# Kernel optimization log

Hardware: AMD Instinct MI355X
Metric: run time of the kernel (lower is better)

Reference implementation:

```python
import jax, jax.numpy as jnp
import numpy as np

# Video-DiT scale: d_model = H * D = 2048
B, S_T, S_C, H, D = 2, 2048, 1024, 16, 128


def setup_inputs() -> dict:
    key = jax.random.key(0)
    ks = jax.random.split(key, 6)
    f = lambda k, s: jax.random.normal(k, s, dtype=jnp.float32)
    return {
        "target_q": f(ks[0], (B, S_T, H, D)),
        "target_k": f(ks[1], (B, S_T, H, D)),
        "target_v": f(ks[2], (B, S_T, H, D)),
        "cond_k": f(ks[3], (B, S_C, H, D)),
        "cond_v": f(ks[4], (B, S_C, H, D)),
        "b_param": f(ks[5], (1,)),
    }


def reference(target_q, target_k, target_v, cond_k, cond_v, b_param):
    """Extended target self-attention over [target_k; cond_k] with a scalar
    logit bias b_param added only to the condition-key columns.
    Inputs BSHD; returns [B, S_t, H*D] (ready for output_proj)."""
    Bq, St, Hh, Dd = target_q.shape
    Sc = cond_k.shape[1]
    scale = Dd ** -0.5  # softmax_scale defaults to head_dim**-0.5

    k_ext = jnp.concatenate([target_k, cond_k], axis=1)  # [B, S_t+S_c, H, D]
    v_ext = jnp.concatenate([target_v, cond_v], axis=1)

    # [B, H, S_t, S_t+S_c]
    logits = jnp.einsum('bqhd,bkhd->bhqk', target_q, k_ext) * jnp.asarray(scale, target_q.dtype)
    # bias: 0 on target keys, b on cond keys
    bias = jnp.concatenate([
        jnp.zeros((St,), logits.dtype),
        jnp.broadcast_to(b_param.astype(logits.dtype), (Sc,)),
    ])
    logits = logits + bias[None, None, None, :]

    probs = jax.nn.softmax(logits, axis=-1)
    out = jnp.einsum('bhqk,bkhd->bqhd', probs, v_ext)  # [B, S_t, H, D]
    return out.reshape(Bq, St, Hh * Dd)
```

## Files before the change

kernel.cpp:

```cpp
#include <hip/hip_runtime.h>
#include <hip/hip_bf16.h>

typedef __attribute__((ext_vector_type(4))) float f32x4;
typedef __attribute__((ext_vector_type(16))) float f32x16;
typedef __attribute__((ext_vector_type(8))) short bf8;
typedef __attribute__((ext_vector_type(2))) int i32x2;

#define B_ 2
#define ST 2048
#define SC 1024
#define SK 3072
#define NH 16
#define DH 128
#define KVB 32
#define NT 96
#define TGT 64
#define SCALE 0.088388347648318447f
#define LOG2E 1.4426950408889634f

__device__ __forceinline__ i32x2 tr_read(unsigned a) {
    i32x2 d;
    asm volatile("ds_read_b64_tr_b16 %0, %1" : "=v"(d) : "v"(a));
    return d;
}

__device__ __forceinline__ unsigned cvtpk(float lo, float hi) {
    unsigned r;
    asm("v_cvt_pk_bf16_f32 %0, %1, %2" : "=v"(r) : "v"(lo), "v"(hi));
    return r;
}

__device__ __forceinline__ void swap32(unsigned &a, unsigned &b) {
    asm volatile("v_permlane32_swap_b32 %0, %1" : "+v"(a), "+v"(b));
}

__device__ __forceinline__ bf8 mk_bf8(i32x2 a, i32x2 b) {
    union { i32x2 h[2]; bf8 v; } u;
    u.h[0] = a; u.h[1] = b;
    return u.v;
}
__device__ __forceinline__ bf8 mk_bf8w(unsigned w0, unsigned w1, unsigned w2, unsigned w3) {
    union { unsigned w[4]; bf8 v; } u;
    u.w[0] = w0; u.w[1] = w1; u.w[2] = w2; u.w[3] = w3;
    return u.v;
}
__device__ __forceinline__ bf8 pack_bf8(f32x4 a, f32x4 b) {
    return mk_bf8w(cvtpk(a[0], a[1]), cvtpk(a[2], a[3]),
                   cvtpk(b[0], b[1]), cvtpk(b[2], b[3]));
}

__global__ __launch_bounds__(256, 2)
void attn_fwd(const float* __restrict__ Q,
              const float* __restrict__ TK,
              const float* __restrict__ TV,
              const float* __restrict__ CK,
              const float* __restrict__ CV,
              const float* __restrict__ BP,
              float* __restrict__ OUT)
{
    __shared__ __align__(16) unsigned short Ks[2][KVB * DH];
    __shared__ __align__(16) unsigned short Vs[2][KVB * DH];

    const int tid = threadIdx.x;
    const int w   = tid >> 6;
    const int l   = tid & 63;
    const int r31 = l & 31;
    const int hi  = l >> 5;

    const int bid = blockIdx.x;
    const int xcd = bid & 7;
    const int sub = bid >> 3;
    const int bh  = xcd * 4 + (sub >> 4);
    const int qt  = sub & 15;
    const int bb  = bh >> 4;
    const int hh  = bh & 15;

    const float biasl = BP[0] * LOG2E;

    const int qrow = qt * 128 + w * 32 + r31;
    const float* qp = Q + (((size_t)bb * ST + qrow) * NH + hh) * DH;
    const float qsc = SCALE * LOG2E;
    bf8 qf[8];
#pragma unroll
    for (int dk = 0; dk < 8; ++dk) {
        const f32x4 x0 = *(const f32x4*)(qp + dk * 16 + hi * 8);
        const f32x4 x1 = *(const f32x4*)(qp + dk * 16 + hi * 8 + 4);
        qf[dk] = mk_bf8w(cvtpk(x0[0]*qsc, x0[1]*qsc), cvtpk(x0[2]*qsc, x0[3]*qsc),
                         cvtpk(x1[0]*qsc, x1[1]*qsc), cvtpk(x1[2]*qsc, x1[3]*qsc));
    }

    f32x16 oa[4];
#pragma unroll
    for (int dt = 0; dt < 4; ++dt)
#pragma unroll
        for (int e = 0; e < 16; ++e) oa[dt][e] = 0.f;
    float l_run = 0.f;

    f32x4 skr[2][2], svr[2][2];

    auto stage_load = [&](int t) {
        const int kv0 = t * KVB;
        const float *kb, *vb;
        if (kv0 < ST) {
            const size_t off = (((size_t)bb * ST + kv0) * NH + hh) * DH;
            kb = TK + off; vb = TV + off;
        } else {
            const size_t off = (((size_t)bb * SC + (kv0 - ST)) * NH + hh) * DH;
            kb = CK + off; vb = CV + off;
        }
#pragma unroll
        for (int i = 0; i < 2; ++i) {
            const int c = tid + (i << 8);
            const int krow = c >> 4;
            const int kcol = ((c & 15) ^ (krow & 7)) << 3;
            const float* kp = kb + (size_t)krow * (NH * DH) + kcol;
            skr[i][0] = *(const f32x4*)kp;
            skr[i][1] = *(const f32x4*)(kp + 4);
            const int vkv = (((c >> 8) & 1) << 4) | (((c >> 4) & 1) << 3)
                          | (((c >> 7) & 1) << 2) | ((c >> 1) & 3);
            const int vd  = (((c >> 5) & 3) << 5) | (((c >> 3) & 1) << 4)
                          | ((c & 1) << 3);
            const float* vp = vb + (size_t)vkv * (NH * DH) + vd;
            svr[i][0] = *(const f32x4*)vp;
            svr[i][1] = *(const f32x4*)(vp + 4);
        }
    };

    auto stage_write = [&](int buf) {
#pragma unroll
        for (int i = 0; i < 2; ++i) {
            const int c = tid + (i << 8);
            *(bf8*)((char*)Ks[buf] + c * 16) = pack_bf8(skr[i][0], skr[i][1]);
            *(bf8*)((char*)Vs[buf] + c * 16) = pack_bf8(svr[i][0], svr[i][1]);
        }
    };

    stage_load(0);
    stage_write(0);

    const unsigned vLane = (unsigned)(size_t)&Vs[0][0]
                         + (unsigned)((l >> 4) * 128 + (l & 15) * 8);

    for (int t = 0; t < NT; ++t) {
        __syncthreads();
        if (t + 1 < NT) stage_load(t + 1);
        const int buf = t & 1;
        const float bias = (t >= TGT) ? biasl : 0.f;

        f32x16 s0;
#pragma unroll
        for (int e = 0; e < 16; ++e) s0[e] = bias;
        __builtin_amdgcn_s_setprio(1);
#pragma unroll
        for (int dk = 0; dk < 8; ++dk) {
            int o = r31 * 256 + (dk * 16 + hi * 8) * 2;
            o ^= (r31 & 7) << 4;
            const bf8 kf = *(const bf8*)((const char*)Ks[buf] + o);
            s0 = __builtin_amdgcn_mfma_f32_32x32x16_bf16(kf, qf[dk], s0, 0, 0, 0);
        }
        __builtin_amdgcn_s_setprio(0);

        asm volatile("" ::: "memory");
        const unsigned vA = vLane + (unsigned)(buf << 13);
        i32x2 vt_[2][4][2];
#pragma unroll
        for (int ks = 0; ks < 2; ++ks) {
            const unsigned vk = vA + (unsigned)(ks << 12);
#pragma unroll
            for (int dt = 0; dt < 4; ++dt) {
                vt_[ks][dt][0] = tr_read(vk + dt * 512);
                vt_[ks][dt][1] = tr_read(vk + dt * 512 + 2048);
            }
        }

        if (t + 1 < NT) stage_write(buf ^ 1);

        float rs = 0.f;
#pragma unroll
        for (int e = 0; e < 16; ++e) {
            s0[e] = __builtin_amdgcn_exp2f(s0[e]);
            rs += s0[e];
        }
        l_run += rs;

        unsigned a0 = cvtpk(s0[0], s0[1]),  b0 = cvtpk(s0[4], s0[5]);
        unsigned a1 = cvtpk(s0[2], s0[3]),  b1 = cvtpk(s0[6], s0[7]);
        swap32(a0, b0); swap32(a1, b1);
        const bf8 pf0 = mk_bf8w(a0, a1, b0, b1);
        unsigned a2 = cvtpk(s0[8], s0[9]),   b2 = cvtpk(s0[12], s0[13]);
        unsigned a3 = cvtpk(s0[10], s0[11]), b3 = cvtpk(s0[14], s0[15]);
        swap32(a2, b2); swap32(a3, b3);
        const bf8 pf1 = mk_bf8w(a2, a3, b2, b3);

        asm volatile("s_waitcnt lgkmcnt(0)");
        __builtin_amdgcn_sched_barrier(0);
        __builtin_amdgcn_s_setprio(1);
#pragma unroll
        for (int ks = 0; ks < 2; ++ks) {
            const bf8 pf = ks ? pf1 : pf0;
#pragma unroll
            for (int dt = 0; dt < 4; ++dt) {
                const bf8 vf = mk_bf8(vt_[ks][dt][0], vt_[ks][dt][1]);
                oa[dt] = __builtin_amdgcn_mfma_f32_32x32x16_bf16(vf, pf, oa[dt], 0, 0, 0);
            }
        }
        __builtin_amdgcn_s_setprio(0);
    }

    const float l_tot = l_run + __shfl_xor(l_run, 32);
    const float inv = 1.0f / l_tot;
    float* op = OUT + ((size_t)(bb * ST + qrow)) * (NH * DH) + hh * DH;
#pragma unroll
    for (int dt = 0; dt < 4; ++dt)
#pragma unroll
        for (int rr = 0; rr < 4; ++rr) {
            f32x4 st;
            st[0] = oa[dt][rr * 4 + 0] * inv;
            st[1] = oa[dt][rr * 4 + 1] * inv;
            st[2] = oa[dt][rr * 4 + 2] * inv;
            st[3] = oa[dt][rr * 4 + 3] * inv;
            *(f32x4*)(op + dt * 32 + rr * 8 + hi * 4) = st;
        }
}

extern "C" void kernel_launch(void* const* d_in, const int* in_sizes, int n_in,
                              void* d_out, int out_size, void* d_ws, size_t ws_size,
                              hipStream_t stream) {
    const float* q  = (const float*)d_in[0];
    const float* tk = (const float*)d_in[1];
    const float* tv = (const float*)d_in[2];
    const float* ck = (const float*)d_in[3];
    const float* cv = (const float*)d_in[4];
    const float* bp = (const float*)d_in[5];
    float* out = (float*)d_out;
    attn_fwd<<<dim3((ST / 128) * B_ * NH), 256, 0, stream>>>(q, tk, tv, ck, cv, bp, out);
}
```

Measured before the change: 141.3 us.

## Pre-convert K/V to swizzled bf16 tiles and stream them via global_load_lds

Adds a preconversion kernel that converts K and V from fp32 into bf16, laid out in the swizzled per-tile order the attention kernel expects, and stores them in the workspace. The attention kernel then copies each tile straight into LDS with global_load_lds. This removes the repeated fp32 loads, conversions and LDS stores that each of the 16 query-tile blocks per head did before. The cost is an extra kernel launch and a full read and write pass over K/V. It falls back to the old kernel when the workspace is too small.

```diff
diff --git a/kernel.cpp b/kernel.cpp
--- a/kernel.cpp
+++ b/kernel.cpp
@@ -17,6 +17,9 @@
 #define TGT 64
 #define SCALE 0.088388347648318447f
 #define LOG2E 1.4426950408889634f
+#define PRE_TILE_U32 2048
+#define PRE_BYTES (32ull * 96 * 512 * 16)
+#define WS_NEED (2ull * PRE_BYTES)
 
 __device__ __forceinline__ i32x2 tr_read(unsigned a) {
     i32x2 d;
@@ -49,14 +52,204 @@
                    cvtpk(b[0], b[1]), cvtpk(b[2], b[3]));
 }
 
+__global__ __launch_bounds__(256)
+void preconv(const float* __restrict__ TK, const float* __restrict__ TV,
+             const float* __restrict__ CK, const float* __restrict__ CV,
+             unsigned* __restrict__ KP, unsigned* __restrict__ VP)
+{
+    const unsigned gid = blockIdx.x * 256 + threadIdx.x;
+    const int c    = gid & 511;
+    const int idx  = gid >> 9;
+    const int bhid = idx / 96;
+    const int t    = idx - bhid * 96;
+    const int bb   = bhid >> 4;
+    const int hh   = bhid & 15;
+
+    const int krow = c >> 4;
+    const int kcol = ((c & 15) ^ (krow & 7)) << 3;
+    const int gkv  = t * 32 + krow;
+    const float* kp = (gkv < ST)
+        ? TK + (((size_t)bb * ST + gkv) * NH + hh) * DH + kcol
+        : CK + (((size_t)bb * SC + (gkv - ST)) * NH + hh) * DH + kcol;
+    const f32x4 k0 = *(const f32x4*)kp;
+    const f32x4 k1 = *(const f32x4*)(kp + 4);
+    unsigned* ko = KP + (size_t)gid * 4;
+    ko[0] = cvtpk(k0[0], k0[1]); ko[1] = cvtpk(k0[2], k0[3]);
+    ko[2] = cvtpk(k1[0], k1[1]); ko[3] = cvtpk(k1[2], k1[3]);
+
+    const int vkv = (((c >> 8) & 1) << 4) | (((c >> 4) & 1) << 3)
+                  | (((c >> 7) & 1) << 2) | ((c >> 1) & 3);
+    const int vd  = (((c >> 5) & 3) << 5) | (((c >> 3) & 1) << 4)
+                  | ((c & 1) << 3);
+    const int gvv = t * 32 + vkv;
+    const float* vp = (gvv < ST)
+        ? TV + (((size_t)bb * ST + gvv) * NH + hh) * DH + vd
+        : CV + (((size_t)bb * SC + (gvv - ST)) * NH + hh) * DH + vd;
+    const f32x4 v0 = *(const f32x4*)vp;
+    const f32x4 v1 = *(const f32x4*)(vp + 4);
+    unsigned* vo = VP + (size_t)gid * 4;
+    vo[0] = cvtpk(v0[0], v0[1]); vo[1] = cvtpk(v0[2], v0[3]);
+    vo[2] = cvtpk(v1[0], v1[1]); vo[3] = cvtpk(v1[2], v1[3]);
+}
+
 __global__ __launch_bounds__(256, 2)
-void attn_fwd(const float* __restrict__ Q,
-              const float* __restrict__ TK,
-              const float* __restrict__ TV,
-              const float* __restrict__ CK,
-              const float* __restrict__ CV,
-              const float* __restrict__ BP,
-              float* __restrict__ OUT)
+void attn_fwd_pre(const float* __restrict__ Q,
+                  const unsigned* __restrict__ KP,
+                  const unsigned* __restrict__ VP,
+                  const float* __restrict__ BP,
+                  float* __restrict__ OUT)
+{
+    __shared__ __align__(16) unsigned short Ks[2][KVB * DH];
+    __shared__ __align__(16) unsigned short Vs[2][KVB * DH];
+
+    const int tid = threadIdx.x;
+    const int w   = tid >> 6;
+    const int l   = tid & 63;
+    const int r31 = l & 31;
+    const int hi  = l >> 5;
+
+    const int bid = blockIdx.x;
+    const int xcd = bid & 7;
+    const int sub = bid >> 3;
+    const int bh  = xcd * 4 + (sub >> 4);
+    const int qt  = sub & 15;
+    const int bb  = bh >> 4;
+    const int hh  = bh & 15;
+    const int bh96 = bh * 96;
+
+    const float biasl = BP[0] * LOG2E;
+
+    const int qrow = qt * 128 + w * 32 + r31;
+    const float* qp = Q + (((size_t)bb * ST + qrow) * NH + hh) * DH;
+    const float qsc = SCALE * LOG2E;
+    bf8 qf[8];
+#pragma unroll
+    for (int dk = 0; dk < 8; ++dk) {
+        const f32x4 x0 = *(const f32x4*)(qp + dk * 16 + hi * 8);
+        const f32x4 x1 = *(const f32x4*)(qp + dk * 16 + hi * 8 + 4);
+        qf[dk] = mk_bf8w(cvtpk(x0[0]*qsc, x0[1]*qsc), cvtpk(x0[2]*qsc, x0[3]*qsc),
+                         cvtpk(x1[0]*qsc, x1[1]*qsc), cvtpk(x1[2]*qsc, x1[3]*qsc));
+    }
+
+    f32x16 oa[4];
+#pragma unroll
+    for (int dt = 0; dt < 4; ++dt)
+#pragma unroll
+        for (int e = 0; e < 16; ++e) oa[dt][e] = 0.f;
+    float l_run = 0.f;
+
+    auto stage = [&](int t, int buf) {
+        const unsigned* kt = KP + (size_t)(bh96 + t) * PRE_TILE_U32;
+        const unsigned* vt = VP + (size_t)(bh96 + t) * PRE_TILE_U32;
+#pragma unroll
+        for (int i = 0; i < 2; ++i) {
+            const int cb = (w << 6) + (i << 8);
+            const unsigned kdst = (unsigned)(size_t)&Ks[buf][cb * 8];
+            const unsigned vdst = (unsigned)(size_t)&Vs[buf][cb * 8];
+            const unsigned* kg = kt + (size_t)(cb + l) * 4;
+            const unsigned* vg = vt + (size_t)(cb + l) * 4;
+            __builtin_amdgcn_global_load_lds(
+                (const __attribute__((address_space(1))) unsigned*)(size_t)kg,
+                (__attribute__((address_space(3))) unsigned*)(size_t)kdst, 16, 0, 0);
+            __builtin_amdgcn_global_load_lds(
+                (const __attribute__((address_space(1))) unsigned*)(size_t)vg,
+                (__attribute__((address_space(3))) unsigned*)(size_t)vdst, 16, 0, 0);
+        }
+    };
+
+    stage(0, 0);
+
+    const unsigned vLane = (unsigned)(size_t)&Vs[0][0]
+                         + (unsigned)((l >> 4) * 128 + (l & 15) * 8);
+
+    for (int t = 0; t < NT; ++t) {
+        __syncthreads();
+        if (t + 1 < NT) stage(t + 1, (t ^ 1) & 1);
+        const int buf = t & 1;
+        const float bias = (t >= TGT) ? biasl : 0.f;
+
+        f32x16 s0;
+#pragma unroll
+        for (int e = 0; e < 16; ++e) s0[e] = bias;
+        __builtin_amdgcn_s_setprio(1);
+#pragma unroll
+        for (int dk = 0; dk < 8; ++dk) {
+            int o = r31 * 256 + (dk * 16 + hi * 8) * 2;
+            o ^= (r31 & 7) << 4;
+            const bf8 kf = *(const bf8*)((const char*)Ks[buf] + o);
+            s0 = __builtin_amdgcn_mfma_f32_32x32x16_bf16(kf, qf[dk], s0, 0, 0, 0);
+        }
+        __builtin_amdgcn_s_setprio(0);
+
+        asm volatile("" ::: "memory");
+        const unsigned vA = vLane + (unsigned)(buf << 13);
+        i32x2 vt_[2][4][2];
+#pragma unroll
+        for (int ks = 0; ks < 2; ++ks) {
+            const unsigned vk = vA + (unsigned)(ks << 12);
+#pragma unroll
+            for (int dt = 0; dt < 4; ++dt) {
+                vt_[ks][dt][0] = tr_read(vk + dt * 512);
+                vt_[ks][dt][1] = tr_read(vk + dt * 512 + 2048);
+            }
+        }
+
+        float rs = 0.f;
+#pragma unroll
+        for (int e = 0; e < 16; ++e) {
+            s0[e] = __builtin_amdgcn_exp2f(s0[e]);
+            rs += s0[e];
+        }
+        l_run += rs;
+
+        unsigned a0 = cvtpk(s0[0], s0[1]),  b0 = cvtpk(s0[4], s0[5]);
+        unsigned a1 = cvtpk(s0[2], s0[3]),  b1 = cvtpk(s0[6], s0[7]);
+        swap32(a0, b0); swap32(a1, b1);
+        const bf8 pf0 = mk_bf8w(a0, a1, b0, b1);
+        unsigned a2 = cvtpk(s0[8], s0[9]),   b2 = cvtpk(s0[12], s0[13]);
+        unsigned a3 = cvtpk(s0[10], s0[11]), b3 = cvtpk(s0[14], s0[15]);
+        swap32(a2, b2); swap32(a3, b3);
+        const bf8 pf1 = mk_bf8w(a2, a3, b2, b3);
+
+        asm volatile("s_waitcnt lgkmcnt(0)");
+        __builtin_amdgcn_sched_barrier(0);
+        __builtin_amdgcn_s_setprio(1);
+#pragma unroll
+        for (int ks = 0; ks < 2; ++ks) {
+            const bf8 pf = ks ? pf1 : pf0;
+#pragma unroll
+            for (int dt = 0; dt < 4; ++dt) {
+                const bf8 vf = mk_bf8(vt_[ks][dt][0], vt_[ks][dt][1]);
+                oa[dt] = __builtin_amdgcn_mfma_f32_32x32x16_bf16(vf, pf, oa[dt], 0, 0, 0);
+            }
+        }
+        __builtin_amdgcn_s_setprio(0);
+    }
+
+    const float l_tot = l_run + __shfl_xor(l_run, 32);
+    const float inv = 1.0f / l_tot;
+    float* op = OUT + ((size_t)(bb * ST + qrow)) * (NH * DH) + hh * DH;
+#pragma unroll
+    for (int dt = 0; dt < 4; ++dt)
+#pragma unroll
+        for (int rr = 0; rr < 4; ++rr) {
+            f32x4 st;
+            st[0] = oa[dt][rr * 4 + 0] * inv;
+            st[1] = oa[dt][rr * 4 + 1] * inv;
+            st[2] = oa[dt][rr * 4 + 2] * inv;
+            st[3] = oa[dt][rr * 4 + 3] * inv;
+            *(f32x4*)(op + dt * 32 + rr * 8 + hi * 4) = st;
+        }
+}
+
+__global__ __launch_bounds__(256, 2)
+void attn_fwd_reg(const float* __restrict__ Q,
+                  const float* __restrict__ TK,
+                  const float* __restrict__ TV,
+                  const float* __restrict__ CK,
+                  const float* __restrict__ CV,
+                  const float* __restrict__ BP,
+                  float* __restrict__ OUT)
 {
     __shared__ __align__(16) unsigned short Ks[2][KVB * DH];
     __shared__ __align__(16) unsigned short Vs[2][KVB * DH];
@@ -125,7 +318,6 @@
             svr[i][1] = *(const f32x4*)(vp + 4);
         }
     };
-
     auto stage_write = [&](int buf) {
 #pragma unroll
         for (int i = 0; i < 2; ++i) {
@@ -233,5 +425,13 @@
     const float* cv = (const float*)d_in[4];
     const float* bp = (const float*)d_in[5];
     float* out = (float*)d_out;
-    attn_fwd<<<dim3((ST / 128) * B_ * NH), 256, 0, stream>>>(q, tk, tv, ck, cv, bp, out);
-}
+
+    if (ws_size >= WS_NEED) {
+        unsigned* kp = (unsigned*)d_ws;
+        unsigned* vp = (unsigned*)((char*)d_ws + PRE_BYTES);
+        preconv<<<dim3(6144), 256, 0, stream>>>(tk, tv, ck, cv, kp, vp);
+        attn_fwd_pre<<<dim3(512), 256, 0, stream>>>(q, kp, vp, bp, out);
+    } else {
+        attn_fwd_reg<<<dim3(512), 256, 0, stream>>>(q, tk, tv, ck, cv, bp, out);
+    }
+}
```

Result: slower. 146.1 us (+3.4%).
